# Performance work log

Hardware: AMD Instinct MI355X
Metric: run time of the kernel (lower is better)

The kernel has to match this reference:

```python
import jax, jax.numpy as jnp
import numpy as np
from jax import lax

GROUPS = 32
CH = 2048
CG = CH // GROUPS  # 64 channels per group
H = W = 64
B = 4
EPS = 1e-5


def _conv2d(x, w, b, padding, dilation=1):
    # x: [N, Cin, H, W], w: [Cout, Cin, kh, kw] (OIHW)
    y = lax.conv_general_dilated(
        x, w, window_strides=(1, 1),
        padding=[(padding, padding), (padding, padding)],
        rhs_dilation=(dilation, dilation),
        dimension_numbers=("NCHW", "OIHW", "NCHW"))
    return y + b[None, :, None, None]


def _prelu(x, alpha):
    # single shared slope (num_parameters=1)
    return jnp.where(x >= 0, x, alpha[0] * x)


def setup_inputs() -> dict:
    key = jax.random.key(0)
    ks = jax.random.split(key, 6)
    s = 0.05
    f32 = jnp.float32
    return {
        "x": jax.random.normal(ks[0], (B, CH, H, W), f32),
        # EFFM.conv1x1 (on concatenated pooled h/w strips)
        "w_hw": jax.random.normal(ks[1], (CG, CG, 1, 1), f32) * s,
        "b_hw": jnp.zeros((CG,), f32),
        # GroupNorm(cg, cg): per-channel affine
        "gn_w": jnp.ones((CG,), f32),
        "gn_b": jnp.zeros((CG,), f32),
        # RC branch1: 3x3 conv pad=1 + PReLU
        "w_b1": jax.random.normal(ks[2], (CG, CG, 3, 3), f32) * s,
        "b_b1": jnp.zeros((CG,), f32),
        "a_b1": jnp.full((1,), 0.25, f32),
        # RC branch2: 3x3 conv dilation=2 pad=2 + PReLU
        "w_b2": jax.random.normal(ks[3], (CG, CG, 3, 3), f32) * s,
        "b_b2": jnp.zeros((CG,), f32),
        "a_b2": jnp.full((1,), 0.25, f32),
        # RC conv128to64: 1x1 conv 2*cg -> cg
        "w_cat": jax.random.normal(ks[4], (CG, 2 * CG, 1, 1), f32) * s,
        "b_cat": jnp.zeros((CG,), f32),
    }


def _effm(x, w_hw, b_hw, gn_w, gn_b, w_b1, b_b1, a_b1, w_b2, b_b2, a_b2, w_cat, b_cat):
    b, c, h, w = x.shape
    cg = c // GROUPS
    bg = b * GROUPS
    gx = x.reshape(bg, cg, h, w)

    # --- coordinate attention branch ---
    x_h = jnp.mean(gx, axis=3, keepdims=True)                       # [bg, cg, h, 1]
    x_w = jnp.mean(gx, axis=2, keepdims=True).transpose(0, 1, 3, 2)  # [bg, cg, w, 1]
    hw = jnp.concatenate([x_h, x_w], axis=2)                         # [bg, cg, h+w, 1]
    # 1x1 conv == channel mixing linear
    hw = jnp.einsum("oi,bilk->bolk", w_hw[:, :, 0, 0], hw) + b_hw[None, :, None, None]
    x_h, x_w = hw[:, :, :h, :], hw[:, :, h:, :]
    gate = gx * jax.nn.sigmoid(x_h) * jax.nn.sigmoid(x_w.transpose(0, 1, 3, 2))

    # GroupNorm(num_groups=cg, num_channels=cg) == per-channel instance norm
    mu = jnp.mean(gate, axis=(2, 3), keepdims=True)
    var = jnp.var(gate, axis=(2, 3), keepdims=True)
    x1 = (gate - mu) * lax.rsqrt(var + EPS)
    x1 = x1 * gn_w[None, :, None, None] + gn_b[None, :, None, None]

    # --- RC multi-scale branch ---
    br1 = _prelu(_conv2d(gx, w_b1, b_b1, padding=1), a_b1) + gx
    br2 = _prelu(_conv2d(gx, w_b2, b_b2, padding=2, dilation=2), a_b2) + gx
    cat = jnp.concatenate([br1, br2], axis=1)                        # [bg, 2cg, h, w]
    x2 = jnp.einsum("oi,bihw->bohw", w_cat[:, :, 0, 0], cat) + b_cat[None, :, None, None]

    # --- cross softmax-matmul attention ---
    x11 = jax.nn.softmax(jnp.mean(x1, axis=(2, 3)), axis=-1)          # [bg, cg]
    x21 = jax.nn.softmax(jnp.mean(x2, axis=(2, 3)), axis=-1)          # [bg, cg]
    weights = (jnp.einsum("gc,gchw->ghw", x11, x2)
               + jnp.einsum("gc,gchw->ghw", x21, x1))                # [bg, h, w]
    out = gx * jax.nn.sigmoid(weights)[:, None, :, :]
    return out.reshape(b, c, h, w)


def reference(x, w_hw, b_hw, gn_w, gn_b, w_b1, b_b1, a_b1, w_b2, b_b2, a_b2, w_cat, b_cat):
    return _effm(x, w_hw, b_hw, gn_w, gn_b, w_b1, b_b1, a_b1, w_b2, b_b2, a_b2, w_cat, b_cat)
```

## Files before the change

kernel.cpp:

```cpp
#include <hip/hip_runtime.h>
#include <hip/hip_bf16.h>

#define HWPX 4096

typedef __attribute__((ext_vector_type(8))) short short8v;
typedef __attribute__((ext_vector_type(4))) float f32x4;
typedef __attribute__((ext_vector_type(16))) float f32x16;
#define MFMA32(a,b,c) __builtin_amdgcn_mfma_f32_32x32x16_bf16(a,b,c,0,0,0)

__device__ __forceinline__ float sigf(float x){ return 1.0f/(1.0f+__expf(-x)); }
__device__ __forceinline__ unsigned short f2bf(float f){
  __hip_bfloat16 h = __float2bfloat16(f);
  unsigned short u; __builtin_memcpy(&u, &h, sizeof(u)); return u;
}
__device__ __forceinline__ float bf2f(unsigned short u){
  return __uint_as_float(((unsigned)u)<<16);
}
__device__ __forceinline__ void gl2lds16(const void* g, void* l){
  __builtin_amdgcn_global_load_lds((const __attribute__((address_space(1))) void*)g,
                                   (__attribute__((address_space(3))) void*)l, 16, 0, 0);
}

__global__ __launch_bounds__(256) void k_pre(const float* __restrict__ x,
                                             const float* __restrict__ wb1,
                                             const float* __restrict__ wb2,
                                             const float* __restrict__ wcat,
                                             const float* __restrict__ gnb,
                                             unsigned short* __restrict__ xb,
                                             float* __restrict__ hwbuf,
                                             unsigned short* __restrict__ wimg,
                                             unsigned short* __restrict__ wcimg,
                                             float* __restrict__ x11,
                                             float* __restrict__ x2mean){
  int bid = blockIdx.x, tid = threadIdx.x;
  if (bid >= 1088){
    int idx = (bid - 1088)*2048 + tid*8;
    f32x4 z = {0.f,0.f,0.f,0.f};
    *(f32x4*)(x2mean + idx) = z;
    *(f32x4*)(x2mean + idx + 4) = z;
    return;
  }
  if (bid >= 1024){
    int bid2 = bid - 1024;
    for (int idx = bid2*256 + tid; idx < 73728; idx += 64*256){
      int f = idx >> 9, r = idx & 511, lane = r >> 3, j = r & 7;
      int qc = f / 36, rem = f % 36, tap = rem >> 2, kc = rem & 3;
      int q = qc >> 1, conv = qc & 1, kf = kc >> 1, cot = kc & 1;
      int co = cot*32 + (lane & 31);
      int ci = q*32 + kf*16 + (lane >> 5)*8 + j;
      const float* src = conv ? wb2 : wb1;
      wimg[idx] = f2bf(src[(co*64 + ci)*9 + tap]);
    }
    if (bid2 == 0){
      for (int idx = tid; idx < 8192; idx += 256){
        int f = idx >> 9, r = idx & 511, lane = r >> 3, j = r & 7;
        int kfc = f >> 1, cot = f & 1;
        int o = cot*32 + (lane & 31);
        int ch = kfc*16 + (lane >> 5)*8 + j;
        wcimg[idx] = f2bf(wcat[o*128 + ch]);
      }
      if (tid < 64){
        float g = gnb[tid];
        float m = g;
        for (int s=32; s; s>>=1) m = fmaxf(m, __shfl_xor(m, s));
        float e = __expf(g-m);
        float se = e;
        for (int s=32; s; s>>=1) se += __shfl_xor(se, s);
        x11[tid] = e/se;
      }
    }
    return;
  }
  int g = bid >> 3, slot = bid & 7;
  int col = tid & 63, wid = tid >> 6;
  __shared__ float rsm[8*64];
  __shared__ float csm[4*8*64];
  float colacc[8] = {0,0,0,0,0,0,0,0};
  const float* xbase = x + ((size_t)(g*64 + slot*8))*HWPX;
  for (int p=0;p<16;++p){
    int r = wid + 4*p;
    const float* src = xbase + r*64 + col;
    float v[8];
    #pragma unroll
    for (int e=0;e<8;e++) v[e] = src[(size_t)e*HWPX];
    unsigned pk[4];
    #pragma unroll
    for (int j=0;j<4;j++) pk[j] = (unsigned)f2bf(v[2*j]) | ((unsigned)f2bf(v[2*j+1])<<16);
    f32x4 st; __builtin_memcpy(&st, pk, 16);
    *(f32x4*)((char*)xb + (((size_t)(g*64+r))*8 + slot)*1024 + col*16) = st;
    #pragma unroll
    for (int e=0;e<8;e++){
      float s = v[e];
      s += __shfl_xor(s,1); s += __shfl_xor(s,2); s += __shfl_xor(s,4);
      s += __shfl_xor(s,8); s += __shfl_xor(s,16); s += __shfl_xor(s,32);
      if ((tid&63)==0) rsm[e*64+r] = s;
      colacc[e] += v[e];
    }
  }
  #pragma unroll
  for (int e=0;e<8;e++) csm[(wid*8+e)*64+col] = colacc[e];
  __syncthreads();
  float* hb = hwbuf + ((size_t)(g*64 + slot*8))*128;
  for (int idx=tid; idx<512; idx+=256){
    int e = idx>>6, r = idx&63;
    hb[e*128 + r] = rsm[e*64+r] * (1.0f/64.0f);
  }
  for (int idx=tid; idx<512; idx+=256){
    int e = idx>>6, c2 = idx&63;
    float s = csm[(0*8+e)*64+c2] + csm[(1*8+e)*64+c2] + csm[(2*8+e)*64+c2] + csm[(3*8+e)*64+c2];
    hb[e*128 + 64 + c2] = s * (1.0f/64.0f);
  }
}

__global__ __launch_bounds__(256) void k_hwmm(const float* hwbuf, const float* whw,
                                              const float* bhw, float* sigbuf){
  int g = blockIdx.x;
  __shared__ float hl[64*128];
  int tid = threadIdx.x;
  const float* src = hwbuf + (size_t)g*8192;
  for (int i = tid; i < 2048; i += 256) ((float4*)hl)[i] = ((const float4*)src)[i];
  __syncthreads();
  int p  = tid & 127;
  int o0 = (tid >> 7) * 32;
  float acc[32];
  #pragma unroll
  for (int k=0;k<32;k++) acc[k] = bhw[o0+k];
  for (int i=0;i<64;i++){
    float v = hl[i*128+p];
    #pragma unroll
    for (int k=0;k<32;k++) acc[k] = fmaf(whw[(o0+k)*64+i], v, acc[k]);
  }
  float* dst = sigbuf + (size_t)g*8192;
  #pragma unroll
  for (int k=0;k<32;k++) dst[(o0+k)*128+p] = sigf(acc[k]);
}

__global__ __launch_bounds__(256) void k_gate2(const unsigned short* __restrict__ xb,
                                               const float* __restrict__ sigbuf,
                                               const float* __restrict__ gnw,
                                               const float* __restrict__ gnb,
                                               float* __restrict__ scsh){
  int bsw = blockIdx.x;
  int g = bsw >> 3, slot = bsw & 7;
  int tid = threadIdx.x, col = tid & 63, wq = tid >> 6, lane = tid & 63;
  __shared__ float srm[8*64], scm[8*64], red[4*16];
  for (int idx = tid; idx < 1024; idx += 256){
    int e = idx >> 7, k = idx & 127;
    float v = sigbuf[(size_t)g*8192 + (size_t)(slot*8+e)*128 + k];
    if (k < 64) srm[e*64+k] = v; else scm[e*64+k-64] = v;
  }
  __syncthreads();
  float s[8] = {0,0,0,0,0,0,0,0}, s2[8] = {0,0,0,0,0,0,0,0};
  const char* base = (const char*)xb + (((size_t)(g*64))*8 + slot)*1024;
  for (int p=0;p<16;++p){
    int row = wq*16 + p;
    short8v xv = *(const short8v*)(base + (size_t)row*8192 + col*16);
    #pragma unroll
    for (int e=0;e<8;e++){
      float v = bf2f((unsigned short)xv[e]) * srm[e*64+row] * scm[e*64+col];
      s[e] += v; s2[e] = fmaf(v, v, s2[e]);
    }
  }
  #pragma unroll
  for (int e=0;e<8;e++){
    #pragma unroll
    for (int off=1; off<64; off<<=1){ s[e] += __shfl_xor(s[e], off); s2[e] += __shfl_xor(s2[e], off); }
  }
  if (lane == 0){
    #pragma unroll
    for (int e=0;e<8;e++){ red[wq*16+e] = s[e]; red[wq*16+8+e] = s2[e]; }
  }
  __syncthreads();
  if (tid < 8){
    float S  = red[tid]   + red[16+tid] + red[32+tid] + red[48+tid];
    float S2 = red[8+tid] + red[24+tid] + red[40+tid] + red[56+tid];
    float mu = S*(1.f/4096.f);
    float var = S2*(1.f/4096.f) - mu*mu;
    int c = slot*8 + tid;
    float scale = rsqrtf(var + 1e-5f) * gnw[c];
    scsh[(g*64+c)*2]   = scale;
    scsh[(g*64+c)*2+1] = gnb[c] - mu*scale;
  }
}

__global__ __launch_bounds__(512) void k_convcat(const unsigned short* __restrict__ xb,
                                                 const char* __restrict__ wgl,
                                                 const char* __restrict__ wcgl,
                                                 const float* __restrict__ bb1,
                                                 const float* __restrict__ bb2,
                                                 const float* __restrict__ a1p,
                                                 const float* __restrict__ a2p,
                                                 const float* __restrict__ bcat,
                                                 const float* __restrict__ x11,
                                                 float* __restrict__ wsum2,
                                                 float* __restrict__ x2mean){
  extern __shared__ char smem[];
  char* INL = smem;
  char* WL  = smem + 52224;
  char* BRL = smem;
  char* WCL = smem + 131072;
  float* x11l = (float*)(smem + 147456);
  float* bcl  = x11l + 64;

  const int tid = threadIdx.x;
  const int bsw = blockIdx.x;
  const int g = bsw >> 3;
  const int strip = bsw & 7;
  const int r0 = strip*8;
  const int w = tid >> 6;
  const int lane = tid & 63;
  const int l31 = lane & 31;
  const int lh  = lane >> 5;
  const int conv = w >> 2;
  const int ch2 = (w >> 1) & 1;
  const int rquad = w & 1;
  const int dil = conv + 1;

  #pragma unroll
  for (int k=0;k<2;k++){
    int idx = tid + k*512;
    gl2lds16(wcgl + (size_t)idx*16, WCL + idx*16);
  }
  if (tid < 64){ x11l[tid] = x11[tid]; bcl[tid] = bcat[tid]; }
  if (tid < 192){
    int seg = tid >> 2, pc = tid & 3;
    int colp = (pc < 2) ? pc : pc + 64;
    *(f32x4*)(INL + seg*1088 + colp*16) = (f32x4){0.f,0.f,0.f,0.f};
  }

  f32x16 acc[2][4];
  #pragma unroll
  for (int cot=0;cot<2;cot++)
    #pragma unroll
    for (int pt=0;pt<4;pt++)
      #pragma unroll
      for (int e=0;e<16;e++) acc[cot][pt][e] = 0.f;

  for (int q=0;q<2;++q){
    if (q) __syncthreads();
    #pragma unroll
    for (int k=0;k<9;k++){
      int idx = tid + k*512;
      gl2lds16(wgl + (size_t)q*73728 + (size_t)idx*16, WL + idx*16);
    }
    #pragma unroll
    for (int i=0;i<6;++i){
      int seg = w*6 + i;
      int row = seg >> 2, slot = seg & 3;
      int rg = r0 - 2 + row;
      char* dst = INL + seg*1088 + 32;
      if ((unsigned)rg < 64u){
        const char* src = (const char*)xb + ((((size_t)(g*64+rg))*8) + q*4 + slot)*1024 + lane*16;
        gl2lds16(src, dst + lane*16);
      } else {
        *(f32x4*)(dst + lane*16) = (f32x4){0.f,0.f,0.f,0.f};
      }
    }
    __syncthreads();
    #pragma unroll
    for (int tap=0;tap<9;++tap){
      const int dy = tap/3 - 1, dx = tap%3 - 1;
      #pragma unroll
      for (int kf=0;kf<2;++kf){
        const char* wp = WL + (size_t)(((conv*9+tap)*4 + kf*2)*1024) + lane*16;
        short8v A0 = *(const short8v*)(wp);
        short8v A1 = *(const short8v*)(wp + 1024);
        const char* ib = INL + (kf*2 + lh)*1088 + (ch2*32 + 2 + l31 + dx*dil)*16;
        #pragma unroll
        for (int pt=0;pt<4;++pt){
          int rowin = rquad*4 + pt + dy*dil + 2;
          short8v B = *(const short8v*)(ib + rowin*4352);
          acc[0][pt] = MFMA32(A0, B, acc[0][pt]);
          acc[1][pt] = MFMA32(A1, B, acc[1][pt]);
        }
      }
    }
  }
  __syncthreads();

  {
    const float alpha = conv ? a2p[0] : a1p[0];
    const float* bbp = conv ? bb2 : bb1;
    #pragma unroll
    for (int cot=0;cot<2;++cot){
      #pragma unroll
      for (int rq=0;rq<4;++rq){
        int co0 = cot*32 + 8*rq + 4*lh;
        float b0 = bbp[co0], b1 = bbp[co0+1], b2 = bbp[co0+2], b3 = bbp[co0+3];
        int ch0 = conv*64 + co0;
        #pragma unroll
        for (int pt=0;pt<4;++pt){
          int prow = rquad*4 + pt;
          int colg = ch2*32 + l31;
          const char* rsrc = (const char*)xb + (((size_t)(g*64 + r0 + prow))*8 + (co0>>3))*1024
                             + colg*16 + (co0&7)*2;
          ushort4 rv = *(const ushort4*)rsrc;
          float v0 = acc[cot][pt][rq*4+0] + b0; v0 = (v0>=0.f? v0 : alpha*v0) + bf2f(rv.x);
          float v1 = acc[cot][pt][rq*4+1] + b1; v1 = (v1>=0.f? v1 : alpha*v1) + bf2f(rv.y);
          float v2 = acc[cot][pt][rq*4+2] + b2; v2 = (v2>=0.f? v2 : alpha*v2) + bf2f(rv.z);
          float v3 = acc[cot][pt][rq*4+3] + b3; v3 = (v3>=0.f? v3 : alpha*v3) + bf2f(rv.w);
          int px = prow*64 + colg;
          int addr = (px*256 + ch0*2) ^ ((px & 15) << 4);
          ushort4 pk; pk.x=f2bf(v0); pk.y=f2bf(v1); pk.z=f2bf(v2); pk.w=f2bf(v3);
          *(ushort4*)(BRL + addr) = pk;
        }
      }
    }
  }
  __syncthreads();

  {
    f32x16 c2[2][2];
    #pragma unroll
    for (int cot=0;cot<2;cot++)
      #pragma unroll
      for (int t=0;t<2;t++)
        #pragma unroll
        for (int e=0;e<16;e++) c2[cot][t][e] = 0.f;

    #pragma unroll
    for (int kfc=0;kfc<8;++kfc){
      const char* ap = WCL + (size_t)(kfc*2)*1024 + lane*16;
      short8v A0 = *(const short8v*)(ap);
      short8v A1 = *(const short8v*)(ap + 1024);
      #pragma unroll
      for (int t=0;t<2;++t){
        int px = w*64 + t*32 + l31;
        int addr = (px*256 + kfc*32 + lh*16) ^ ((px & 15) << 4);
        short8v B = *(const short8v*)(BRL + addr);
        c2[0][t] = MFMA32(A0, B, c2[0][t]);
        c2[1][t] = MFMA32(A1, B, c2[1][t]);
      }
    }
    float u0 = 0.f, u1 = 0.f;
    #pragma unroll
    for (int cot=0;cot<2;++cot){
      #pragma unroll
      for (int reg=0;reg<16;++reg){
        int o = cot*32 + (reg&3) + 8*(reg>>2) + 4*lh;
        float xw = x11l[o], bc = bcl[o];
        u0 += xw*(c2[cot][0][reg] + bc);
        u1 += xw*(c2[cot][1][reg] + bc);
        float sv = c2[cot][0][reg] + c2[cot][1][reg];
        sv += __shfl_xor(sv, 1); sv += __shfl_xor(sv, 2);
        sv += __shfl_xor(sv, 4); sv += __shfl_xor(sv, 8); sv += __shfl_xor(sv, 16);
        if (l31 == 0) atomicAdd(&x2mean[g*64 + o], sv);
      }
    }
    u0 += __shfl_xor(u0, 32);
    u1 += __shfl_xor(u1, 32);
    if (lh == 0){
      float* wp2 = wsum2 + (size_t)g*4096 + strip*512 + w*64 + l31;
      wp2[0]  = u0;
      wp2[32] = u1;
    }
  }
}

__global__ __launch_bounds__(256) void k_final2(const float* __restrict__ x,
                                                const float* __restrict__ sigbuf,
                                                const float* __restrict__ scsh,
                                                const float* __restrict__ x2mean,
                                                const float* __restrict__ bcat,
                                                const float* __restrict__ wsum2,
                                                float* __restrict__ out){
  int blk = blockIdx.x;
  int g = blk >> 4, chunk = blk & 15;
  int tid = threadIdx.x;
  __shared__ float x21s[64];
  __shared__ float crow[64*4];
  __shared__ float ccol[64*64];
  __shared__ float Ssm;
  const float* sgb = sigbuf + (size_t)g*8192;
  if (tid < 64){
    float mean = x2mean[g*64 + tid] * (1.f/4096.f) + bcat[tid];
    float mx = mean;
    for (int s=32; s; s>>=1) mx = fmaxf(mx, __shfl_xor(mx, s));
    float e = __expf(mean - mx);
    float se = e;
    for (int s=32; s; s>>=1) se += __shfl_xor(se, s);
    x21s[tid] = e/se;
  }
  for (int idx = tid; idx < 4096; idx += 256){
    int c = idx >> 6, col = idx & 63;
    ccol[idx] = sgb[c*128 + 64 + col];
  }
  __syncthreads();
  {
    int c = tid >> 2, rr = tid & 3;
    crow[tid] = x21s[c] * scsh[(g*64+c)*2] * sgb[c*128 + chunk*4 + rr];
  }
  if (tid < 64){
    float v = x21s[tid] * scsh[(g*64+tid)*2+1];
    for (int s=32; s; s>>=1) v += __shfl_xor(v, s);
    if (tid == 0) Ssm = v;
  }
  __syncthreads();
  int px = chunk*256 + tid;
  int rr = tid >> 6, col = tid & 63;
  const float* xp = x + (size_t)(g*64)*HWPX + px;
  float W = wsum2[(size_t)g*4096 + px] + Ssm;
  float xv[64];
  #pragma unroll
  for (int c=0;c<64;c++){
    xv[c] = xp[(size_t)c*HWPX];
    W = fmaf(crow[c*4+rr]*ccol[c*64+col], xv[c], W);
  }
  float s = sigf(W);
  float* op = out + (size_t)(g*64)*HWPX + px;
  #pragma unroll
  for (int c=0;c<64;c++){
    op[(size_t)c*HWPX] = xv[c] * s;
  }
}

extern "C" void kernel_launch(void* const* d_in, const int* in_sizes, int n_in,
                              void* d_out, int out_size, void* d_ws, size_t ws_size,
                              hipStream_t stream) {
  const float* x     = (const float*)d_in[0];
  const float* w_hw  = (const float*)d_in[1];
  const float* b_hw  = (const float*)d_in[2];
  const float* gn_w  = (const float*)d_in[3];
  const float* gn_b  = (const float*)d_in[4];
  const float* w_b1  = (const float*)d_in[5];
  const float* b_b1  = (const float*)d_in[6];
  const float* a_b1  = (const float*)d_in[7];
  const float* w_b2  = (const float*)d_in[8];
  const float* b_b2  = (const float*)d_in[9];
  const float* a_b2  = (const float*)d_in[10];
  const float* w_cat = (const float*)d_in[11];
  const float* b_cat = (const float*)d_in[12];

  char* ws = (char*)d_ws;
  unsigned short* wimg  = (unsigned short*)(ws + 0);
  unsigned short* wcimg = (unsigned short*)(ws + 147456);
  float* x11    = (float*)(ws + 163840);
  float* x2mean = (float*)(ws + 164096);
  float* scsh   = (float*)(ws + 196864);
  float* wsum2  = (float*)(ws + 262400);
  float* hwbuf  = (float*)(ws + 2359552);
  float* sigb   = (float*)(ws + 6553856);
  unsigned short* xb = (unsigned short*)d_out;
  float* out = (float*)d_out;

  hipFuncSetAttribute(reinterpret_cast<const void*>(k_convcat),
                      hipFuncAttributeMaxDynamicSharedMemorySize, 147968);

  k_pre  <<<1092, 256, 0, stream>>>(x, w_b1, w_b2, w_cat, gn_b, xb, hwbuf, wimg, wcimg,
                                    x11, x2mean);
  k_hwmm <<<128,  256, 0, stream>>>(hwbuf, w_hw, b_hw, sigb);
  k_gate2<<<1024, 256, 0, stream>>>(xb, sigb, gn_w, gn_b, scsh);
  k_convcat<<<1024, 512, 147968, stream>>>(xb, (const char*)wimg, (const char*)wcimg,
                                           b_b1, b_b2, a_b1, a_b2, b_cat, x11, wsum2, x2mean);
  k_final2<<<2048, 256, 0, stream>>>(x, sigb, scsh, x2mean, b_cat, wsum2, out);
}
```

Baseline: 275.5 us.

## Split convcat output tiles across 1024 threads and read bf16 input in final pass

k_convcat now launches 1024 threads and gives each wave one 32-channel output tile instead of two. This halves per-thread accumulator registers and doubles the waves available to hide latency. The second half of the 1x1 reduction goes to a new wsum2b buffer, which k_final2 sums. k_final2 now reads the bf16 channel-packed copy of x, moved from the output buffer into the workspace, instead of fp32 x. This halves the large input read, at the cost of bf16 precision in the final gx*sigmoid product.

```diff
diff --git a/kernel.cpp b/kernel.cpp
--- a/kernel.cpp
+++ b/kernel.cpp
@@ -183,17 +183,18 @@
   }
 }
 
-__global__ __launch_bounds__(512) void k_convcat(const unsigned short* __restrict__ xb,
-                                                 const char* __restrict__ wgl,
-                                                 const char* __restrict__ wcgl,
-                                                 const float* __restrict__ bb1,
-                                                 const float* __restrict__ bb2,
-                                                 const float* __restrict__ a1p,
-                                                 const float* __restrict__ a2p,
-                                                 const float* __restrict__ bcat,
-                                                 const float* __restrict__ x11,
-                                                 float* __restrict__ wsum2,
-                                                 float* __restrict__ x2mean){
+__global__ __launch_bounds__(1024) void k_convcat(const unsigned short* __restrict__ xb,
+                                                  const char* __restrict__ wgl,
+                                                  const char* __restrict__ wcgl,
+                                                  const float* __restrict__ bb1,
+                                                  const float* __restrict__ bb2,
+                                                  const float* __restrict__ a1p,
+                                                  const float* __restrict__ a2p,
+                                                  const float* __restrict__ bcat,
+                                                  const float* __restrict__ x11,
+                                                  float* __restrict__ wsum2,
+                                                  float* __restrict__ wsum2b,
+                                                  float* __restrict__ x2mean){
   extern __shared__ char smem[];
   char* INL = smem;
   char* WL  = smem + 52224;
@@ -203,24 +204,20 @@
   float* bcl  = x11l + 64;
 
   const int tid = threadIdx.x;
-  const int bsw = blockIdx.x;
-  const int g = bsw >> 3;
-  const int strip = bsw & 7;
+  const int g = blockIdx.x >> 3;
+  const int strip = blockIdx.x & 7;
   const int r0 = strip*8;
   const int w = tid >> 6;
   const int lane = tid & 63;
   const int l31 = lane & 31;
   const int lh  = lane >> 5;
-  const int conv = w >> 2;
-  const int ch2 = (w >> 1) & 1;
-  const int rquad = w & 1;
+  const int conv = w >> 3;
+  const int ch2 = (w >> 2) & 1;
+  const int rquad = (w >> 1) & 1;
+  const int cot = w & 1;
   const int dil = conv + 1;
 
-  #pragma unroll
-  for (int k=0;k<2;k++){
-    int idx = tid + k*512;
-    gl2lds16(wcgl + (size_t)idx*16, WCL + idx*16);
-  }
+  gl2lds16(wcgl + (size_t)tid*16, WCL + tid*16);
   if (tid < 64){ x11l[tid] = x11[tid]; bcl[tid] = bcat[tid]; }
   if (tid < 192){
     int seg = tid >> 2, pc = tid & 3;
@@ -228,24 +225,26 @@
     *(f32x4*)(INL + seg*1088 + colp*16) = (f32x4){0.f,0.f,0.f,0.f};
   }
 
-  f32x16 acc[2][4];
-  #pragma unroll
-  for (int cot=0;cot<2;cot++)
-    #pragma unroll
-    for (int pt=0;pt<4;pt++)
-      #pragma unroll
-      for (int e=0;e<16;e++) acc[cot][pt][e] = 0.f;
+  f32x16 acc[4];
+  #pragma unroll
+  for (int pt=0;pt<4;pt++)
+    #pragma unroll
+    for (int e=0;e<16;e++) acc[pt][e] = 0.f;
 
   for (int q=0;q<2;++q){
     if (q) __syncthreads();
     #pragma unroll
-    for (int k=0;k<9;k++){
-      int idx = tid + k*512;
+    for (int k=0;k<4;k++){
+      int idx = tid + k*1024;
       gl2lds16(wgl + (size_t)q*73728 + (size_t)idx*16, WL + idx*16);
     }
-    #pragma unroll
-    for (int i=0;i<6;++i){
-      int seg = w*6 + i;
+    if (tid < 512){
+      int idx = 4096 + tid;
+      gl2lds16(wgl + (size_t)q*73728 + (size_t)idx*16, WL + idx*16);
+    }
+    #pragma unroll
+    for (int i=0;i<3;++i){
+      int seg = w*3 + i;
       int row = seg >> 2, slot = seg & 3;
       int rg = r0 - 2 + row;
       char* dst = INL + seg*1088 + 32;
@@ -262,16 +261,14 @@
       const int dy = tap/3 - 1, dx = tap%3 - 1;
       #pragma unroll
       for (int kf=0;kf<2;++kf){
-        const char* wp = WL + (size_t)(((conv*9+tap)*4 + kf*2)*1024) + lane*16;
+        const char* wp = WL + (size_t)(((conv*9+tap)*4 + kf*2 + cot)*1024) + lane*16;
         short8v A0 = *(const short8v*)(wp);
-        short8v A1 = *(const short8v*)(wp + 1024);
         const char* ib = INL + (kf*2 + lh)*1088 + (ch2*32 + 2 + l31 + dx*dil)*16;
         #pragma unroll
         for (int pt=0;pt<4;++pt){
           int rowin = rquad*4 + pt + dy*dil + 2;
           short8v B = *(const short8v*)(ib + rowin*4352);
-          acc[0][pt] = MFMA32(A0, B, acc[0][pt]);
-          acc[1][pt] = MFMA32(A1, B, acc[1][pt]);
+          acc[pt] = MFMA32(A0, B, acc[pt]);
         }
       }
     }
@@ -282,87 +279,78 @@
     const float alpha = conv ? a2p[0] : a1p[0];
     const float* bbp = conv ? bb2 : bb1;
     #pragma unroll
-    for (int cot=0;cot<2;++cot){
+    for (int rq=0;rq<4;++rq){
+      int co0 = cot*32 + 8*rq + 4*lh;
+      float b0 = bbp[co0], b1 = bbp[co0+1], b2 = bbp[co0+2], b3 = bbp[co0+3];
+      int ch0 = conv*64 + co0;
       #pragma unroll
-      for (int rq=0;rq<4;++rq){
-        int co0 = cot*32 + 8*rq + 4*lh;
-        float b0 = bbp[co0], b1 = bbp[co0+1], b2 = bbp[co0+2], b3 = bbp[co0+3];
-        int ch0 = conv*64 + co0;
-        #pragma unroll
-        for (int pt=0;pt<4;++pt){
-          int prow = rquad*4 + pt;
-          int colg = ch2*32 + l31;
-          const char* rsrc = (const char*)xb + (((size_t)(g*64 + r0 + prow))*8 + (co0>>3))*1024
-                             + colg*16 + (co0&7)*2;
-          ushort4 rv = *(const ushort4*)rsrc;
-          float v0 = acc[cot][pt][rq*4+0] + b0; v0 = (v0>=0.f? v0 : alpha*v0) + bf2f(rv.x);
-          float v1 = acc[cot][pt][rq*4+1] + b1; v1 = (v1>=0.f? v1 : alpha*v1) + bf2f(rv.y);
-          float v2 = acc[cot][pt][rq*4+2] + b2; v2 = (v2>=0.f? v2 : alpha*v2) + bf2f(rv.z);
-          float v3 = acc[cot][pt][rq*4+3] + b3; v3 = (v3>=0.f? v3 : alpha*v3) + bf2f(rv.w);
-          int px = prow*64 + colg;
-          int addr = (px*256 + ch0*2) ^ ((px & 15) << 4);
-          ushort4 pk; pk.x=f2bf(v0); pk.y=f2bf(v1); pk.z=f2bf(v2); pk.w=f2bf(v3);
-          *(ushort4*)(BRL + addr) = pk;
-        }
+      for (int pt=0;pt<4;++pt){
+        int prow = rquad*4 + pt;
+        int colg = ch2*32 + l31;
+        const char* rsrc = (const char*)xb + (((size_t)(g*64 + r0 + prow))*8 + (co0>>3))*1024
+                           + colg*16 + (co0&7)*2;
+        ushort4 rv = *(const ushort4*)rsrc;
+        float v0 = acc[pt][rq*4+0] + b0; v0 = (v0>=0.f? v0 : alpha*v0) + bf2f(rv.x);
+        float v1 = acc[pt][rq*4+1] + b1; v1 = (v1>=0.f? v1 : alpha*v1) + bf2f(rv.y);
+        float v2 = acc[pt][rq*4+2] + b2; v2 = (v2>=0.f? v2 : alpha*v2) + bf2f(rv.z);
+        float v3 = acc[pt][rq*4+3] + b3; v3 = (v3>=0.f? v3 : alpha*v3) + bf2f(rv.w);
+        int px = prow*64 + colg;
+        int addr = (px*256 + ch0*2) ^ ((px & 15) << 4);
+        ushort4 pk; pk.x=f2bf(v0); pk.y=f2bf(v1); pk.z=f2bf(v2); pk.w=f2bf(v3);
+        *(ushort4*)(BRL + addr) = pk;
       }
     }
   }
   __syncthreads();
 
   {
-    f32x16 c2[2][2];
-    #pragma unroll
-    for (int cot=0;cot<2;cot++)
+    f32x16 c2[2];
+    #pragma unroll
+    for (int t=0;t<2;t++)
       #pragma unroll
-      for (int t=0;t<2;t++)
-        #pragma unroll
-        for (int e=0;e<16;e++) c2[cot][t][e] = 0.f;
+      for (int e=0;e<16;e++) c2[t][e] = 0.f;
 
     #pragma unroll
     for (int kfc=0;kfc<8;++kfc){
-      const char* ap = WCL + (size_t)(kfc*2)*1024 + lane*16;
+      const char* ap = WCL + (size_t)(kfc*2 + cot)*1024 + lane*16;
       short8v A0 = *(const short8v*)(ap);
-      short8v A1 = *(const short8v*)(ap + 1024);
       #pragma unroll
       for (int t=0;t<2;++t){
-        int px = w*64 + t*32 + l31;
+        int px = (w>>1)*64 + t*32 + l31;
         int addr = (px*256 + kfc*32 + lh*16) ^ ((px & 15) << 4);
         short8v B = *(const short8v*)(BRL + addr);
-        c2[0][t] = MFMA32(A0, B, c2[0][t]);
-        c2[1][t] = MFMA32(A1, B, c2[1][t]);
+        c2[t] = MFMA32(A0, B, c2[t]);
       }
     }
     float u0 = 0.f, u1 = 0.f;
     #pragma unroll
-    for (int cot=0;cot<2;++cot){
-      #pragma unroll
-      for (int reg=0;reg<16;++reg){
-        int o = cot*32 + (reg&3) + 8*(reg>>2) + 4*lh;
-        float xw = x11l[o], bc = bcl[o];
-        u0 += xw*(c2[cot][0][reg] + bc);
-        u1 += xw*(c2[cot][1][reg] + bc);
-        float sv = c2[cot][0][reg] + c2[cot][1][reg];
-        sv += __shfl_xor(sv, 1); sv += __shfl_xor(sv, 2);
-        sv += __shfl_xor(sv, 4); sv += __shfl_xor(sv, 8); sv += __shfl_xor(sv, 16);
-        if (l31 == 0) atomicAdd(&x2mean[g*64 + o], sv);
-      }
+    for (int reg=0;reg<16;++reg){
+      int o = cot*32 + (reg&3) + 8*(reg>>2) + 4*lh;
+      float xw = x11l[o], bc = bcl[o];
+      u0 += xw*(c2[0][reg] + bc);
+      u1 += xw*(c2[1][reg] + bc);
+      float sv = c2[0][reg] + c2[1][reg];
+      sv += __shfl_xor(sv, 1); sv += __shfl_xor(sv, 2);
+      sv += __shfl_xor(sv, 4); sv += __shfl_xor(sv, 8); sv += __shfl_xor(sv, 16);
+      if (l31 == 0) atomicAdd(&x2mean[g*64 + o], sv);
     }
     u0 += __shfl_xor(u0, 32);
     u1 += __shfl_xor(u1, 32);
     if (lh == 0){
-      float* wp2 = wsum2 + (size_t)g*4096 + strip*512 + w*64 + l31;
+      float* wp2 = (cot ? wsum2b : wsum2) + (size_t)g*4096 + strip*512 + (w>>1)*64 + l31;
       wp2[0]  = u0;
       wp2[32] = u1;
     }
   }
 }
 
-__global__ __launch_bounds__(256) void k_final2(const float* __restrict__ x,
+__global__ __launch_bounds__(256) void k_final2(const unsigned short* __restrict__ xb,
                                                 const float* __restrict__ sigbuf,
                                                 const float* __restrict__ scsh,
                                                 const float* __restrict__ x2mean,
                                                 const float* __restrict__ bcat,
                                                 const float* __restrict__ wsum2,
+                                                const float* __restrict__ wsum2b,
                                                 float* __restrict__ out){
   int blk = blockIdx.x;
   int g = blk >> 4, chunk = blk & 15;
@@ -398,12 +386,18 @@
   __syncthreads();
   int px = chunk*256 + tid;
   int rr = tid >> 6, col = tid & 63;
-  const float* xp = x + (size_t)(g*64)*HWPX + px;
-  float W = wsum2[(size_t)g*4096 + px] + Ssm;
+  int row = chunk*4 + rr;
   float xv[64];
+  const char* xbg = (const char*)xb + (((size_t)(g*64 + row))*8)*1024 + col*16;
+  #pragma unroll
+  for (int slot=0;slot<8;slot++){
+    short8v v8 = *(const short8v*)(xbg + slot*1024);
+    #pragma unroll
+    for (int e=0;e<8;e++) xv[slot*8+e] = bf2f((unsigned short)v8[e]);
+  }
+  float W = wsum2[(size_t)g*4096 + px] + wsum2b[(size_t)g*4096 + px] + Ssm;
   #pragma unroll
   for (int c=0;c<64;c++){
-    xv[c] = xp[(size_t)c*HWPX];
     W = fmaf(crow[c*4+rr]*ccol[c*64+col], xv[c], W);
   }
   float s = sigf(W);
@@ -438,9 +432,10 @@
   float* x2mean = (float*)(ws + 164096);
   float* scsh   = (float*)(ws + 196864);
   float* wsum2  = (float*)(ws + 262400);
-  float* hwbuf  = (float*)(ws + 2359552);
-  float* sigb   = (float*)(ws + 6553856);
-  unsigned short* xb = (unsigned short*)d_out;
+  float* wsum2b = (float*)(ws + 2359552);
+  float* hwbuf  = (float*)(ws + 4456704);
+  float* sigb   = (float*)(ws + 8651008);
+  unsigned short* xb = (unsigned short*)(ws + 16777216);
   float* out = (float*)d_out;
 
   hipFuncSetAttribute(reinterpret_cast<const void*>(k_convcat),
@@ -450,7 +445,8 @@
                                     x11, x2mean);
   k_hwmm <<<128,  256, 0, stream>>>(hwbuf, w_hw, b_hw, sigb);
   k_gate2<<<1024, 256, 0, stream>>>(xb, sigb, gn_w, gn_b, scsh);
-  k_convcat<<<1024, 512, 147968, stream>>>(xb, (const char*)wimg, (const char*)wcimg,
-                                           b_b1, b_b2, a_b1, a_b2, b_cat, x11, wsum2, x2mean);
-  k_final2<<<2048, 256, 0, stream>>>(x, sigb, scsh, x2mean, b_cat, wsum2, out);
-}
+  k_convcat<<<1024, 1024, 147968, stream>>>(xb, (const char*)wimg, (const char*)wcimg,
+                                            b_b1, b_b2, a_b1, a_b2, b_cat, x11,
+                                            wsum2, wsum2b, x2mean);
+  k_final2<<<2048, 256, 0, stream>>>(xb, sigb, scsh, x2mean, b_cat, wsum2, wsum2b, out);
+}
```

After: 271.7 us. Within noise of the previous version (-1.4%).
